# Optimization experiments

Hardware: AMD Instinct MI355X
Metric: run time of the kernel (lower is better)

Reference implementation:

```python
import jax, jax.numpy as jnp
import numpy as np

B, N, C = 4, 1024, 1024
H = 16
D = C // H  # 64
HID = int(int(C * 4.0) * 2 / 3)  # 2730
EPS = 1e-6


def rmsnorm(x, w):
    return x * jax.lax.rsqrt(jnp.mean(x * x, axis=-1, keepdims=True) + EPS) * w


def rope_cos_sin(n, d):
    inv_freq = 1.0 / (10000.0 ** (jnp.arange(0, d, 2, dtype=jnp.float32) / d))
    t = jnp.arange(n, dtype=jnp.float32)
    freqs = jnp.einsum('i,j->ij', t, inv_freq)  # [N, D/2]
    emb = jnp.concatenate([freqs, freqs], axis=-1)  # [N, D]
    return jnp.cos(emb), jnp.sin(emb)


def rotate_half(x):
    x1, x2 = jnp.split(x, 2, axis=-1)
    return jnp.concatenate([-x2, x1], axis=-1)


def setup_inputs() -> dict:
    key = jax.random.key(0)
    ks = jax.random.split(key, 12)
    s = lambda fan_in: 1.0 / np.sqrt(fan_in)
    return {
        'x': jax.random.normal(ks[0], (B, N, C), jnp.float32),
        'c': jax.random.normal(ks[1], (B, C), jnp.float32),
        'norm1_w': jnp.ones((C,), jnp.float32),
        'norm2_w': jnp.ones((C,), jnp.float32),
        'qkv_w': jax.random.normal(ks[2], (C, 3 * C), jnp.float32) * s(C),
        'proj_w': jax.random.normal(ks[3], (C, C), jnp.float32) * s(C),
        'proj_b': jnp.zeros((C,), jnp.float32),
        'qn_w': jnp.ones((D,), jnp.float32),
        'kn_w': jnp.ones((D,), jnp.float32),
        'w1': jax.random.normal(ks[4], (C, HID), jnp.float32) * s(C),
        'w2': jax.random.normal(ks[5], (HID, C), jnp.float32) * s(HID),
        'w3': jax.random.normal(ks[6], (C, HID), jnp.float32) * s(C),
        'ada_w': jax.random.normal(ks[7], (C, 6 * C), jnp.float32) * s(C),
        'ada_b': jnp.zeros((6 * C,), jnp.float32),
    }


def reference(x, c, norm1_w, norm2_w, qkv_w, proj_w, proj_b, qn_w, kn_w, w1, w2, w3, ada_w, ada_b):
    # AdaLN modulation params from conditioning
    mods = jax.nn.silu(c) @ ada_w + ada_b  # [B, 6C]
    sh_msa, sc_msa, g_msa, sh_mlp, sc_mlp, g_mlp = jnp.split(mods, 6, axis=-1)

    # --- attention branch ---
    x_mod = rmsnorm(x, norm1_w) * (1 + sc_msa[:, None, :]) + sh_msa[:, None, :]
    qkv = (x_mod @ qkv_w).reshape(B, N, 3, H, D).transpose(2, 0, 3, 1, 4)  # [3,B,H,N,D]
    q, k, v = qkv[0], qkv[1], qkv[2]
    q = rmsnorm(q, qn_w)
    k = rmsnorm(k, kn_w)
    cos, sin = rope_cos_sin(N, D)  # [N, D]
    q = q * cos + rotate_half(q) * sin
    k = k * cos + rotate_half(k) * sin
    attn = jax.nn.softmax(jnp.einsum('bhqd,bhkd->bhqk', q, k) * (D ** -0.5), axis=-1)
    o = jnp.einsum('bhqk,bhkd->bhqd', attn, v).transpose(0, 2, 1, 3).reshape(B, N, C)
    x = x + g_msa[:, None, :] * (o @ proj_w + proj_b)

    # --- SwiGLU MLP branch ---
    x_mod = rmsnorm(x, norm2_w) * (1 + sc_mlp[:, None, :]) + sh_mlp[:, None, :]
    mlp = (jax.nn.silu(x_mod @ w1) * (x_mod @ w3)) @ w2
    x = x + g_mlp[:, None, :] * mlp
    return x
```

## Files before the change

kernel.cpp:

```cpp
#include <hip/hip_runtime.h>
#include <hip/hip_bf16.h>
#include <stdint.h>

using bf16 = __hip_bfloat16;
using bf16x8 = __attribute__((ext_vector_type(8))) short;
using f32x4  = __attribute__((ext_vector_type(4))) float;
using short4v = __attribute__((ext_vector_type(4))) short;

#define EPSF 1e-6f

__device__ __forceinline__ unsigned short f2bu(float x) {
  union { bf16 h; unsigned short u; } cvt;
  cvt.h = __float2bfloat16(x);
  return cvt.u;
}

typedef __attribute__((address_space(3))) void as3_void;
typedef const __attribute__((address_space(1))) void as1_void;

__device__ __forceinline__ void gload_lds16(const void* g, void* l) {
  as1_void* gp = (as1_void*)(uintptr_t)g;
  as3_void* lp = (as3_void*)(uint32_t)(uintptr_t)l;
  __builtin_amdgcn_global_load_lds(gp, lp, 16, 0, 0);
}

__global__ void rope_tab(float* __restrict__ cosT, float* __restrict__ sinT) {
  const int i = blockIdx.x * 256 + threadIdx.x;
  const int n = i >> 5, fi = i & 31;
  const float invf = powf(10000.f, -(float)fi * (1.f / 32.f));
  const float ang = (float)n * invf;
  cosT[i] = cosf(ang);
  sinT[i] = sinf(ang);
}

__global__ void __launch_bounds__(256) ada_part(const float* __restrict__ cc,
                                                const float* __restrict__ adaw,
                                                float* __restrict__ part) {
  __shared__ float sc[256];
  __shared__ float red[1024];
  const int t = threadIdx.x;
  const int cb = blockIdx.x % 48, ks = blockIdx.x / 48;
  const int k0 = ks * 64;
  {
    const int b = t >> 6, kk = t & 63;
    const float v = cc[b * 1024 + k0 + kk];
    sc[t] = v / (1.f + __expf(-v));
  }
  __syncthreads();
  const int colL = t & 127, kh = t >> 7;
  const int col = cb * 128 + colL;
  float a0 = 0.f, a1 = 0.f, a2 = 0.f, a3 = 0.f;
  const float* ap = adaw + (size_t)(k0 + kh * 32) * 6144 + col;
#pragma unroll
  for (int k = 0; k < 32; ++k) {
    const float awv = ap[(size_t)k * 6144];
    const int kk = kh * 32 + k;
    a0 += sc[kk] * awv; a1 += sc[64 + kk] * awv;
    a2 += sc[128 + kk] * awv; a3 += sc[192 + kk] * awv;
  }
  red[kh * 512 + 0 * 128 + colL] = a0;
  red[kh * 512 + 1 * 128 + colL] = a1;
  red[kh * 512 + 2 * 128 + colL] = a2;
  red[kh * 512 + 3 * 128 + colL] = a3;
  __syncthreads();
  if (kh == 0) {
#pragma unroll
    for (int b = 0; b < 4; ++b) {
      const float s = red[b * 128 + colL] + red[512 + b * 128 + colL];
      part[(size_t)(ks * 4 + b) * 6144 + col] = s;
    }
  }
}

__global__ void __launch_bounds__(256) ada_reduce(const float* __restrict__ part,
                                                  const float* __restrict__ adab,
                                                  float* __restrict__ mods) {
  const int i = blockIdx.x * 256 + threadIdx.x;
  const int b = i / 6144, col = i % 6144;
  float s = adab[col];
#pragma unroll
  for (int ks = 0; ks < 16; ++ks) s += part[(size_t)(ks * 4 + b) * 6144 + col];
  mods[b * 6144 + col] = s;
}

__global__ void __launch_bounds__(256) norm_mod(const float* __restrict__ X,
                                                const float* __restrict__ wgt,
                                                const float* __restrict__ mods,
                                                int sh_off, int sc_off,
                                                bf16* __restrict__ Y) {
  __shared__ float red[4];
  const int row = blockIdx.x, t = threadIdx.x, l = t & 63, wv = t >> 6;
  const float4 xv = ((const float4*)(X + (size_t)row * 1024))[t];
  float ss = xv.x * xv.x + xv.y * xv.y + xv.z * xv.z + xv.w * xv.w;
#pragma unroll
  for (int off = 1; off < 64; off <<= 1) ss += __shfl_xor(ss, off);
  if (l == 0) red[wv] = ss;
  __syncthreads();
  ss = (red[0] + red[1]) + (red[2] + red[3]);
  const float rs = rsqrtf(ss * (1.f / 1024.f) + EPSF);
  const int b = row >> 10;
  const float* mb = mods + b * 6144;
  const int c0 = t * 4;
  float vals[4] = {xv.x, xv.y, xv.z, xv.w};
  short4v yv;
#pragma unroll
  for (int j = 0; j < 4; j++) {
    const int cc = c0 + j;
    const float y = vals[j] * rs * wgt[cc] * (1.f + mb[sc_off + cc]) + mb[sh_off + cc];
    yv[j] = (short)f2bu(y);
  }
  *(short4v*)(Y + (size_t)row * 1024 + c0) = yv;
}

__global__ void __launch_bounds__(256) transpose_all(const float* __restrict__ qkvw,
                                                     const float* __restrict__ projw,
                                                     const float* __restrict__ w1,
                                                     const float* __restrict__ w3,
                                                     const float* __restrict__ w2,
                                                     bf16* __restrict__ qkvwt,
                                                     bf16* __restrict__ projwt,
                                                     bf16* __restrict__ w1t,
                                                     bf16* __restrict__ w3t,
                                                     bf16* __restrict__ w2t) {
  int id = blockIdx.x;
  const float* src; bf16* dst; int R, Cc, ldd, nbx;
  if (id < 3072)      { src = qkvw;  dst = qkvwt;  R = 1024; Cc = 3072; ldd = 1024; nbx = 96; }
  else if ((id -= 3072) < 1024) { src = projw; dst = projwt; R = 1024; Cc = 1024; ldd = 1024; nbx = 32; }
  else if ((id -= 1024) < 2752) { src = w1;    dst = w1t;    R = 1024; Cc = 2730; ldd = 1024; nbx = 86; }
  else if ((id -= 2752) < 2752) { src = w3;    dst = w3t;    R = 1024; Cc = 2730; ldd = 1024; nbx = 86; }
  else                { id -= 2752; src = w2;    dst = w2t;    R = 2730; Cc = 1024; ldd = 2816; nbx = 32; }
  const int bx = id % nbx, by = id / nbx;
  __shared__ float tile[32][33];
  const int tx = threadIdx.x & 31, ty = threadIdx.x >> 5;
  const int ct = bx * 32, rt = by * 32;
#pragma unroll
  for (int kk = 0; kk < 4; ++kk) {
    const int r = rt + ty + kk * 8;
    float v = 0.f;
    if (r < R && (ct + tx) < Cc) v = src[(size_t)r * Cc + ct + tx];
    tile[ty + kk * 8][tx] = v;
  }
  __syncthreads();
#pragma unroll
  for (int kk = 0; kk < 4; ++kk) {
    const int c = ct + ty + kk * 8;
    const int r = rt + tx;
    if (c < Cc && r < ldd) dst[(size_t)c * ldd + r] = __float2bfloat16(tile[tx][ty + kk * 8]);
  }
}

template <int TN, int EPI>
__global__ void __launch_bounds__(256, 3) gemm_p(const bf16* __restrict__ A, int lda,
                                                 const bf16* __restrict__ Bt, int ldb,
                                                 int K, int Nreal, int ldc,
                                                 bf16* __restrict__ outb,
                                                 float* __restrict__ outf,
                                                 const float* __restrict__ resid,
                                                 const float* __restrict__ gate,
                                                 const float* __restrict__ bias) {
  constexpr int BUFSZ = 8192 + TN * 64;
  constexpr int WN = (TN == 128) ? 2 : 1;
  constexpr int MI = (TN == 128) ? 4 : 2;
  constexpr int WTM = (TN == 128) ? 64 : 32;
  __shared__ char smB[3 * BUFSZ];
  const int t = threadIdx.x, l = t & 63, w = t >> 6;
  const int g = l >> 4, cl = l & 15;
  const int cpx = gridDim.x >> 3;
  const int wg = blockIdx.x;
  const int swz0 = (wg & 7) * cpx + (wg >> 3);
  const int m0 = (swz0 & 31) * 128, n0 = (swz0 >> 5) * TN;
  const int wm = w / WN, wn = w % WN;
  f32x4 acc[MI][4] = {};
  const int NK = K >> 5;
  const int srow = t >> 2;
  const int scol = (((t & 3) ^ ((t >> 3) & 3))) * 8;
  const int rsw = (cl >> 1) & 3;

  auto stage = [&](int kt, int buf) {
    char* dst = smB + buf * BUFSZ;
    const int kk = kt * 32 + scol;
    gload_lds16(A + (size_t)(m0 + srow) * lda + kk,      dst + t * 16);
    gload_lds16(A + (size_t)(m0 + 64 + srow) * lda + kk, dst + 4096 + t * 16);
    gload_lds16(Bt + (size_t)(n0 + srow) * ldb + kk,     dst + 8192 + t * 16);
    if constexpr (TN == 128)
      gload_lds16(Bt + (size_t)(n0 + 64 + srow) * ldb + kk, dst + 12288 + t * 16);
  };

  stage(0, 0);
  stage(1, 1);
  if constexpr (TN == 128) asm volatile("s_waitcnt vmcnt(4)" ::: "memory");
  else                     asm volatile("s_waitcnt vmcnt(3)" ::: "memory");
  __builtin_amdgcn_s_barrier();
  __builtin_amdgcn_sched_barrier(0);
  int cur = 0;
  for (int kt = 0; kt < NK; ++kt) {
    if (kt + 2 < NK) stage(kt + 2, (cur >= 1) ? cur - 1 : 2);
    const bf16* Ab = (const bf16*)(smB + cur * BUFSZ);
    const bf16* Bb = (const bf16*)(smB + cur * BUFSZ + 8192);
    bf16x8 af[MI], bfr[4];
#pragma unroll
    for (int i = 0; i < MI; i++)
      af[i] = *(const bf16x8*)&Ab[(wm * WTM + i * 16 + cl) * 32 + ((g ^ rsw) << 3)];
#pragma unroll
    for (int i = 0; i < 4; i++)
      bfr[i] = *(const bf16x8*)&Bb[(wn * 64 + i * 16 + cl) * 32 + ((g ^ rsw) << 3)];
    __builtin_amdgcn_s_setprio(1);
#pragma unroll
    for (int mi = 0; mi < MI; mi++)
#pragma unroll
      for (int ni = 0; ni < 4; ni++)
        acc[mi][ni] = __builtin_amdgcn_mfma_f32_16x16x32_bf16(af[mi], bfr[ni], acc[mi][ni], 0, 0, 0);
    __builtin_amdgcn_s_setprio(0);
    if (kt + 2 < NK) {
      if constexpr (TN == 128) asm volatile("s_waitcnt vmcnt(4)" ::: "memory");
      else                     asm volatile("s_waitcnt vmcnt(3)" ::: "memory");
    } else {
      asm volatile("s_waitcnt vmcnt(0)" ::: "memory");
    }
    __builtin_amdgcn_s_barrier();
    __builtin_amdgcn_sched_barrier(0);
    cur = (cur + 1 == 3) ? 0 : cur + 1;
  }
#pragma unroll
  for (int mi = 0; mi < MI; mi++) {
#pragma unroll
    for (int ni = 0; ni < 4; ni++) {
      const int c = n0 + wn * 64 + ni * 16 + cl;
#pragma unroll
      for (int j = 0; j < 4; j++) {
        const int r = m0 + wm * WTM + mi * 16 + g * 4 + j;
        const float v = acc[mi][ni][j];
        if constexpr (EPI == 0) {
          if (c < Nreal) outb[(size_t)r * ldc + c] = __float2bfloat16(v);
        } else if constexpr (EPI == 1) {
          const int b = r >> 10;
          outf[(size_t)r * ldc + c] = resid[(size_t)r * ldc + c] + gate[b * 6144 + c] * (v + bias[c]);
        } else if constexpr (EPI == 4) {
          const int b = r >> 10;
          outf[(size_t)r * ldc + c] = resid[(size_t)r * ldc + c] + gate[b * 6144 + c] * v;
        }
      }
    }
  }
}

__global__ void __launch_bounds__(256, 3) gemm_qkv(const bf16* __restrict__ A, int lda,
                                                   const bf16* __restrict__ Bt, int ldb,
                                                   const float* __restrict__ cosT,
                                                   const float* __restrict__ sinT,
                                                   const float* __restrict__ qnw,
                                                   const float* __restrict__ knw,
                                                   bf16* __restrict__ Qo,
                                                   bf16* __restrict__ Ko,
                                                   bf16* __restrict__ vbt) {
  constexpr int BUFSZ = 16384;
  __shared__ char smB[3 * BUFSZ];
  const int t = threadIdx.x, l = t & 63, w = t >> 6;
  const int g = l >> 4, cl = l & 15;
  const int cpx = gridDim.x >> 3;
  const int wg = blockIdx.x;
  const int swz0 = (wg & 7) * cpx + (wg >> 3);
  const int m0 = (swz0 & 31) * 128, n0 = (swz0 >> 5) * 128;
  const int wm = w >> 1, wn = w & 1;
  f32x4 acc[4][4] = {};
  const int srow = t >> 2;
  const int scol = (((t & 3) ^ ((t >> 3) & 3))) * 8;
  const int rsw = (cl >> 1) & 3;

  auto stage = [&](int kt, int buf) {
    char* dst = smB + buf * BUFSZ;
    const int kk = kt * 32 + scol;
    gload_lds16(A + (size_t)(m0 + srow) * lda + kk,       dst + t * 16);
    gload_lds16(A + (size_t)(m0 + 64 + srow) * lda + kk,  dst + 4096 + t * 16);
    gload_lds16(Bt + (size_t)(n0 + srow) * ldb + kk,      dst + 8192 + t * 16);
    gload_lds16(Bt + (size_t)(n0 + 64 + srow) * ldb + kk, dst + 12288 + t * 16);
  };

  stage(0, 0);
  stage(1, 1);
  asm volatile("s_waitcnt vmcnt(4)" ::: "memory");
  __builtin_amdgcn_s_barrier();
  __builtin_amdgcn_sched_barrier(0);
  int cur = 0;
  for (int kt = 0; kt < 32; ++kt) {
    if (kt + 2 < 32) stage(kt + 2, (cur >= 1) ? cur - 1 : 2);
    const bf16* Ab = (const bf16*)(smB + cur * BUFSZ);
    const bf16* Bb = (const bf16*)(smB + cur * BUFSZ + 8192);
    bf16x8 af[4], bfr[4];
#pragma unroll
    for (int i = 0; i < 4; i++)
      af[i] = *(const bf16x8*)&Ab[(wm * 64 + i * 16 + cl) * 32 + ((g ^ rsw) << 3)];
#pragma unroll
    for (int i = 0; i < 4; i++)
      bfr[i] = *(const bf16x8*)&Bb[(wn * 64 + i * 16 + cl) * 32 + ((g ^ rsw) << 3)];
    __builtin_amdgcn_s_setprio(1);
#pragma unroll
    for (int mi = 0; mi < 4; mi++)
#pragma unroll
      for (int ni = 0; ni < 4; ni++)
        acc[mi][ni] = __builtin_amdgcn_mfma_f32_16x16x32_bf16(af[mi], bfr[ni], acc[mi][ni], 0, 0, 0);
    __builtin_amdgcn_s_setprio(0);
    if (kt + 2 < 32) asm volatile("s_waitcnt vmcnt(4)" ::: "memory");
    else             asm volatile("s_waitcnt vmcnt(0)" ::: "memory");
    __builtin_amdgcn_s_barrier();
    __builtin_amdgcn_sched_barrier(0);
    cur = (cur + 1 == 3) ? 0 : cur + 1;
  }

  float* cosS = (float*)smB;
  float* sinS = (float*)(smB + 16384);
  const int nb0 = m0 & 1023;
  for (int i = t; i < 4096; i += 256) {
    cosS[i] = cosT[(nb0 + (i >> 5)) * 32 + (i & 31)];
    sinS[i] = sinT[(nb0 + (i >> 5)) * 32 + (i & 31)];
  }
  __syncthreads();

  const int hb = n0 + wn * 64;
  const int type = hb >> 10;
  const int h = (hb & 1023) >> 6;
  const int b = m0 >> 10;
  const int bh = b * 16 + h;

  if (type == 2) {
#pragma unroll
    for (int mi = 0; mi < 4; mi++) {
      const int r0 = m0 + wm * 64 + mi * 16 + g * 4;
      const int nn0 = r0 & 1023;
#pragma unroll
      for (int ni = 0; ni < 4; ni++) {
        const int d = ni * 16 + cl;
        short4v pv;
#pragma unroll
        for (int j = 0; j < 4; j++) pv[j] = (short)f2bu(acc[mi][ni][j]);
        *(short4v*)(vbt + (size_t)bh * 65536 + (size_t)d * 1024 + nn0) = pv;
      }
    }
  } else {
    bf16* dst = (type == 0) ? Qo : Ko;
    const float* nwp = (type == 0) ? qnw : knw;
    const float scale = (type == 0) ? 0.125f : 1.f;
    float wv[4];
#pragma unroll
    for (int ni = 0; ni < 4; ni++) wv[ni] = nwp[ni * 16 + cl];
#pragma unroll
    for (int mi = 0; mi < 4; mi++) {
#pragma unroll
      for (int j = 0; j < 4; j++) {
        float ssq = 0.f;
#pragma unroll
        for (int ni = 0; ni < 4; ni++) ssq += acc[mi][ni][j] * acc[mi][ni][j];
        ssq += __shfl_xor(ssq, 1);
        ssq += __shfl_xor(ssq, 2);
        ssq += __shfl_xor(ssq, 4);
        ssq += __shfl_xor(ssq, 8);
        const float rsn = rsqrtf(ssq * (1.f / 64.f) + EPSF);
        const int r = m0 + wm * 64 + mi * 16 + g * 4 + j;
        const int nn = r & 1023, rr = r - m0;
        float vn[4];
#pragma unroll
        for (int ni = 0; ni < 4; ni++) vn[ni] = acc[mi][ni][j] * rsn * wv[ni];
        const float cs0 = cosS[rr * 32 + cl],      sn0 = sinS[rr * 32 + cl];
        const float cs1 = cosS[rr * 32 + 16 + cl], sn1 = sinS[rr * 32 + 16 + cl];
        const float o0 = (vn[0] * cs0 - vn[2] * sn0) * scale;
        const float o1 = (vn[1] * cs1 - vn[3] * sn1) * scale;
        const float o2 = (vn[2] * cs0 + vn[0] * sn0) * scale;
        const float o3 = (vn[3] * cs1 + vn[1] * sn1) * scale;
        const size_t base = ((size_t)bh * 1024 + nn) * 64;
        dst[base + cl] = __float2bfloat16(o0);
        dst[base + 16 + cl] = __float2bfloat16(o1);
        dst[base + 32 + cl] = __float2bfloat16(o2);
        dst[base + 48 + cl] = __float2bfloat16(o3);
      }
    }
  }
}

__global__ void __launch_bounds__(256, 2) gemm_dual(const bf16* __restrict__ A, int lda,
                                                    const bf16* __restrict__ B1t,
                                                    const bf16* __restrict__ B3t, int ldb,
                                                    int K, int Nreal, int ldc,
                                                    bf16* __restrict__ outb) {
  constexpr int BUFSZ = 24576;
  __shared__ char smB[2 * BUFSZ];
  const int t = threadIdx.x, l = t & 63, w = t >> 6;
  const int g = l >> 4, cl = l & 15;
  const int cpx = gridDim.x >> 3;
  const int wg = blockIdx.x;
  const int swz0 = (wg & 7) * cpx + (wg >> 3);
  const int m0 = (swz0 & 31) * 128, n0 = (swz0 >> 5) * 128;
  const int wm = w >> 1, wn = w & 1;
  f32x4 acc1[4][4] = {}, acc3[4][4] = {};
  const int NK = K >> 5;
  const int srow = t >> 2;
  const int scol = (((t & 3) ^ ((t >> 3) & 3))) * 8;
  const int rsw = (cl >> 1) & 3;

  auto stage = [&](int kt, int buf) {
    char* dst = smB + buf * BUFSZ;
    const int kk = kt * 32 + scol;
    gload_lds16(A   + (size_t)(m0 + srow) * lda + kk,      dst + t * 16);
    gload_lds16(A   + (size_t)(m0 + 64 + srow) * lda + kk, dst + 4096 + t * 16);
    gload_lds16(B1t + (size_t)(n0 + srow) * ldb + kk,      dst + 8192 + t * 16);
    gload_lds16(B1t + (size_t)(n0 + 64 + srow) * ldb + kk, dst + 12288 + t * 16);
    gload_lds16(B3t + (size_t)(n0 + srow) * ldb + kk,      dst + 16384 + t * 16);
    gload_lds16(B3t + (size_t)(n0 + 64 + srow) * ldb + kk, dst + 20480 + t * 16);
  };

  stage(0, 0);
  for (int kt = 0; kt < NK; ++kt) {
    if (kt + 1 < NK) {
      stage(kt + 1, (kt + 1) & 1);
      asm volatile("s_waitcnt vmcnt(6)" ::: "memory");
    } else {
      asm volatile("s_waitcnt vmcnt(0)" ::: "memory");
    }
    __builtin_amdgcn_s_barrier();
    __builtin_amdgcn_sched_barrier(0);
    const bf16* Ab  = (const bf16*)(smB + (kt & 1) * BUFSZ);
    const bf16* B1b = (const bf16*)(smB + (kt & 1) * BUFSZ + 8192);
    const bf16* B3b = (const bf16*)(smB + (kt & 1) * BUFSZ + 16384);
    bf16x8 af[4], b1r[4], b3r[4];
#pragma unroll
    for (int i = 0; i < 4; i++)
      af[i] = *(const bf16x8*)&Ab[(wm * 64 + i * 16 + cl) * 32 + ((g ^ rsw) << 3)];
#pragma unroll
    for (int i = 0; i < 4; i++) {
      b1r[i] = *(const bf16x8*)&B1b[(wn * 64 + i * 16 + cl) * 32 + ((g ^ rsw) << 3)];
      b3r[i] = *(const bf16x8*)&B3b[(wn * 64 + i * 16 + cl) * 32 + ((g ^ rsw) << 3)];
    }
    __builtin_amdgcn_s_setprio(1);
#pragma unroll
    for (int mi = 0; mi < 4; mi++)
#pragma unroll
      for (int ni = 0; ni < 4; ni++) {
        acc1[mi][ni] = __builtin_amdgcn_mfma_f32_16x16x32_bf16(af[mi], b1r[ni], acc1[mi][ni], 0, 0, 0);
        acc3[mi][ni] = __builtin_amdgcn_mfma_f32_16x16x32_bf16(af[mi], b3r[ni], acc3[mi][ni], 0, 0, 0);
      }
    __builtin_amdgcn_s_setprio(0);
    __builtin_amdgcn_s_barrier();
    __builtin_amdgcn_sched_barrier(0);
  }
#pragma unroll
  for (int mi = 0; mi < 4; mi++) {
#pragma unroll
    for (int ni = 0; ni < 4; ni++) {
      const int c = n0 + wn * 64 + ni * 16 + cl;
#pragma unroll
      for (int j = 0; j < 4; j++) {
        const int r = m0 + wm * 64 + mi * 16 + g * 4 + j;
        if (c < Nreal) {
          const float hv = acc1[mi][ni][j];
          const float sl = hv / (1.f + __expf(-hv));
          outb[(size_t)r * ldc + c] = __float2bfloat16(sl * acc3[mi][ni][j]);
        } else {
          outb[(size_t)r * ldc + c] = __float2bfloat16(0.f);
        }
      }
    }
  }
}

__global__ void __launch_bounds__(512) attn_fwd(const bf16* __restrict__ Qb,
                                                const bf16* __restrict__ Kb,
                                                const bf16* __restrict__ Vb,
                                                bf16* __restrict__ Ob) {
  __shared__ char KsB[2 * 8192];
  __shared__ char VsB[2 * 8192];
  __shared__ unsigned short Ps[8 * 16 * 64];
  const int t = threadIdx.x, l = t & 63, w = t >> 6;
  const int g = l >> 4, cl = l & 15;
  const int wg = blockIdx.x;
  const int bh = wg & 63;
  const int q0 = (wg >> 6) * 128;
  const bf16* Qg = Qb + (size_t)bh * 65536;
  const bf16* Kg = Kb + (size_t)bh * 65536;
  const bf16* Vg = Vb + (size_t)bh * 65536;
  const int qrow = q0 + w * 16 + cl;
  const bf16x8 aq0 = *(const bf16x8*)(Qg + (size_t)qrow * 64 + g * 8);
  const bf16x8 aq1 = *(const bf16x8*)(Qg + (size_t)qrow * 64 + 32 + g * 8);
  float mreg = -1e30f, lreg = 0.f;
  f32x4 o[4] = {};
  const int kr_l = t >> 3;
  const int ku = (t & 7) ^ ((t >> 3) & 7);
  unsigned short* Pw = Ps + w * 1024;
  const int sxor = cl & 7;

  auto stageKV = [&](int kvt, int buf) {
    const int kv0 = kvt * 64;
    gload_lds16(Kg + (size_t)(kv0 + kr_l) * 64 + ku * 8, KsB + buf * 8192 + w * 1024);
    gload_lds16(Vg + (size_t)kr_l * 1024 + kv0 + ku * 8, VsB + buf * 8192 + w * 1024);
  };

  stageKV(0, 0);
  for (int kvt = 0; kvt < 16; ++kvt) {
    const int cb = kvt & 1;
    if (kvt + 1 < 16) {
      stageKV(kvt + 1, cb ^ 1);
      asm volatile("s_waitcnt vmcnt(2)" ::: "memory");
    } else {
      asm volatile("s_waitcnt vmcnt(0)" ::: "memory");
    }
    __builtin_amdgcn_s_barrier();
    __builtin_amdgcn_sched_barrier(0);
    const char* Kt = KsB + cb * 8192;
    const char* Vt = VsB + cb * 8192;
    f32x4 s[4] = {};
#pragma unroll
    for (int ch = 0; ch < 4; ch++) {
      const int rb = (16 * ch + cl) << 7;
      const bf16x8 bk0 = *(const bf16x8*)(Kt + rb + ((g ^ sxor) << 4));
      s[ch] = __builtin_amdgcn_mfma_f32_16x16x32_bf16(bk0, aq0, s[ch], 0, 0, 0);
      const bf16x8 bk1 = *(const bf16x8*)(Kt + rb + (((4 + g) ^ sxor) << 4));
      s[ch] = __builtin_amdgcn_mfma_f32_16x16x32_bf16(bk1, aq1, s[ch], 0, 0, 0);
    }
    float pm = fmaxf(fmaxf(fmaxf(s[0][0], s[0][1]), fmaxf(s[0][2], s[0][3])),
                     fmaxf(fmaxf(s[1][0], s[1][1]), fmaxf(s[1][2], s[1][3])));
    pm = fmaxf(pm, fmaxf(fmaxf(fmaxf(s[2][0], s[2][1]), fmaxf(s[2][2], s[2][3])),
                         fmaxf(fmaxf(s[3][0], s[3][1]), fmaxf(s[3][2], s[3][3]))));
    pm = fmaxf(pm, __shfl_xor(pm, 16));
    pm = fmaxf(pm, __shfl_xor(pm, 32));
    const float nm = fmaxf(mreg, pm);
    const float al = __expf(mreg - nm);
    mreg = nm;
    float rs = 0.f;
#pragma unroll
    for (int ch = 0; ch < 4; ch++) {
      const float p0 = __expf(s[ch][0] - nm);
      const float p1 = __expf(s[ch][1] - nm);
      const float p2 = __expf(s[ch][2] - nm);
      const float p3 = __expf(s[ch][3] - nm);
      rs += (p0 + p1) + (p2 + p3);
      short4v pk;
      pk[0] = (short)f2bu(p0); pk[1] = (short)f2bu(p1);
      pk[2] = (short)f2bu(p2); pk[3] = (short)f2bu(p3);
      const int phys = (2 * ch + (g >> 1)) ^ sxor;
      *(short4v*)&Pw[cl * 64 + phys * 8 + 4 * (g & 1)] = pk;
    }
    rs += __shfl_xor(rs, 16);
    rs += __shfl_xor(rs, 32);
    lreg = lreg * al + rs;
#pragma unroll
    for (int dc = 0; dc < 4; dc++) {
      o[dc][0] *= al; o[dc][1] *= al; o[dc][2] *= al; o[dc][3] *= al;
    }
    const bf16x8 pa0 = *(const bf16x8*)&Pw[cl * 64 + ((g ^ sxor) << 3)];
    const bf16x8 pa1 = *(const bf16x8*)&Pw[cl * 64 + (((4 + g) ^ sxor) << 3)];
#pragma unroll
    for (int dc = 0; dc < 4; dc++) {
      const int vr = (16 * dc + cl) << 7;
      const bf16x8 bv0 = *(const bf16x8*)(Vt + vr + ((g ^ sxor) << 4));
      o[dc] = __builtin_amdgcn_mfma_f32_16x16x32_bf16(bv0, pa0, o[dc], 0, 0, 0);
      const bf16x8 bv1 = *(const bf16x8*)(Vt + vr + (((4 + g) ^ sxor) << 4));
      o[dc] = __builtin_amdgcn_mfma_f32_16x16x32_bf16(bv1, pa1, o[dc], 0, 0, 0);
    }
    __builtin_amdgcn_s_barrier();
  }
  const int b = bh >> 4, h = bh & 15;
  const float inv = 1.f / lreg;
  const int q = q0 + w * 16 + cl;
  const size_t base = ((size_t)(b * 1024 + q) * 16 + h) * 64;
#pragma unroll
  for (int dc = 0; dc < 4; dc++) {
    short4v ov;
    ov[0] = (short)f2bu(o[dc][0] * inv);
    ov[1] = (short)f2bu(o[dc][1] * inv);
    ov[2] = (short)f2bu(o[dc][2] * inv);
    ov[3] = (short)f2bu(o[dc][3] * inv);
    *(short4v*)(Ob + base + 16 * dc + 4 * g) = ov;
  }
}

extern "C" void kernel_launch(void* const* d_in, const int* in_sizes, int n_in,
                              void* d_out, int out_size, void* d_ws, size_t ws_size,
                              hipStream_t stream) {
  const float* x     = (const float*)d_in[0];
  const float* c     = (const float*)d_in[1];
  const float* n1w   = (const float*)d_in[2];
  const float* n2w   = (const float*)d_in[3];
  const float* qkvw  = (const float*)d_in[4];
  const float* projw = (const float*)d_in[5];
  const float* projb = (const float*)d_in[6];
  const float* qnw   = (const float*)d_in[7];
  const float* knw   = (const float*)d_in[8];
  const float* w1    = (const float*)d_in[9];
  const float* w2    = (const float*)d_in[10];
  const float* w3    = (const float*)d_in[11];
  const float* adaw  = (const float*)d_in[12];
  const float* adab  = (const float*)d_in[13];
  float* outp = (float*)d_out;
  char* ws = (char*)d_ws;
  if (ws_size < 93159424u) return;

  float* ropeC = (float*)(ws + 0);
  float* ropeS = (float*)(ws + 131072);
  float* mods  = (float*)(ws + 262144);
  bf16* xmod   = (bf16*)(ws + 360448);
  bf16* qkvwt  = (bf16*)(ws + 8749056);
  bf16* projwt = (bf16*)(ws + 15040512);
  bf16* w1t    = (bf16*)(ws + 17137664);
  bf16* w3t    = (bf16*)(ws + 22904832);
  bf16* w2t    = (bf16*)(ws + 28672000);
  float* apart = (float*)(ws + 34439168);
  bf16* qb     = (bf16*)(ws + 59604992);
  bf16* gbuf   = (bf16*)(ws + 59604992);
  bf16* kb     = (bf16*)(ws + 67993600);
  bf16* vbt    = (bf16*)(ws + 76382208);
  bf16* ob     = (bf16*)(ws + 84770816);

  rope_tab<<<128, 256, 0, stream>>>(ropeC, ropeS);
  ada_part<<<768, 256, 0, stream>>>(c, adaw, apart);
  ada_reduce<<<96, 256, 0, stream>>>(apart, adab, mods);
  transpose_all<<<12416, 256, 0, stream>>>(qkvw, projw, w1, w3, w2,
                                           qkvwt, projwt, w1t, w3t, w2t);

  norm_mod<<<4096, 256, 0, stream>>>(x, n1w, mods, 0, 1024, xmod);
  gemm_qkv<<<768, 256, 0, stream>>>(xmod, 1024, qkvwt, 1024, ropeC, ropeS, qnw, knw,
                                    qb, kb, vbt);
  attn_fwd<<<512, 512, 0, stream>>>(qb, kb, vbt, ob);
  gemm_p<64, 1><<<512, 256, 0, stream>>>(ob, 1024, projwt, 1024, 1024, 1024, 1024,
                                         nullptr, outp, x, mods + 2048, projb);

  norm_mod<<<4096, 256, 0, stream>>>(outp, n2w, mods, 3072, 4096, xmod);
  gemm_dual<<<704, 256, 0, stream>>>(xmod, 1024, w1t, w3t, 1024, 1024, 2730, 2816,
                                     gbuf);
  gemm_p<64, 4><<<512, 256, 0, stream>>>(gbuf, 2816, w2t, 2816, 2816, 1024, 1024,
                                         nullptr, outp, outp, mods + 5120, nullptr);
}
```

Measured before the change: 233.9 us.

## Fuse preamble kernels and use exp2 softmax with lazy rescaling

Merges the rope table, adaLN partial matmul and weight transpose/convert kernels into one launch, removing two kernel launches and their serialization gaps. In attention, the log2(e) factor is folded into the Q scale so exp2f replaces __expf. The online-softmax rescale of the accumulator and row sum is skipped unless the running max rises by more than 8 in log2 units. This lazy rescale removes per-iteration multiplies, but lets probabilities reach up to 2^8 before bf16 packing, which could slightly affect accuracy.

```diff
diff --git a/kernel.cpp b/kernel.cpp
--- a/kernel.cpp
+++ b/kernel.cpp
@@ -8,6 +8,7 @@
 using short4v = __attribute__((ext_vector_type(4))) short;
 
 #define EPSF 1e-6f
+#define LOG2E 1.44269504088896f
 
 __device__ __forceinline__ unsigned short f2bu(float x) {
   union { bf16 h; unsigned short u; } cvt;
@@ -24,51 +25,90 @@
   __builtin_amdgcn_global_load_lds(gp, lp, 16, 0, 0);
 }
 
-__global__ void rope_tab(float* __restrict__ cosT, float* __restrict__ sinT) {
-  const int i = blockIdx.x * 256 + threadIdx.x;
-  const int n = i >> 5, fi = i & 31;
-  const float invf = powf(10000.f, -(float)fi * (1.f / 32.f));
-  const float ang = (float)n * invf;
-  cosT[i] = cosf(ang);
-  sinT[i] = sinf(ang);
-}
-
-__global__ void __launch_bounds__(256) ada_part(const float* __restrict__ cc,
+__global__ void __launch_bounds__(256) preamble(const float* __restrict__ qkvw,
+                                                const float* __restrict__ projw,
+                                                const float* __restrict__ w1,
+                                                const float* __restrict__ w3,
+                                                const float* __restrict__ w2,
+                                                bf16* __restrict__ qkvwt,
+                                                bf16* __restrict__ projwt,
+                                                bf16* __restrict__ w1t,
+                                                bf16* __restrict__ w3t,
+                                                bf16* __restrict__ w2t,
+                                                const float* __restrict__ cc,
                                                 const float* __restrict__ adaw,
-                                                float* __restrict__ part) {
+                                                float* __restrict__ part,
+                                                float* __restrict__ cosT,
+                                                float* __restrict__ sinT) {
+  __shared__ float tile[32][33];
   __shared__ float sc[256];
   __shared__ float red[1024];
+  int id = blockIdx.x;
   const int t = threadIdx.x;
-  const int cb = blockIdx.x % 48, ks = blockIdx.x / 48;
-  const int k0 = ks * 64;
-  {
-    const int b = t >> 6, kk = t & 63;
-    const float v = cc[b * 1024 + k0 + kk];
-    sc[t] = v / (1.f + __expf(-v));
-  }
-  __syncthreads();
-  const int colL = t & 127, kh = t >> 7;
-  const int col = cb * 128 + colL;
-  float a0 = 0.f, a1 = 0.f, a2 = 0.f, a3 = 0.f;
-  const float* ap = adaw + (size_t)(k0 + kh * 32) * 6144 + col;
-#pragma unroll
-  for (int k = 0; k < 32; ++k) {
-    const float awv = ap[(size_t)k * 6144];
-    const int kk = kh * 32 + k;
-    a0 += sc[kk] * awv; a1 += sc[64 + kk] * awv;
-    a2 += sc[128 + kk] * awv; a3 += sc[192 + kk] * awv;
-  }
-  red[kh * 512 + 0 * 128 + colL] = a0;
-  red[kh * 512 + 1 * 128 + colL] = a1;
-  red[kh * 512 + 2 * 128 + colL] = a2;
-  red[kh * 512 + 3 * 128 + colL] = a3;
-  __syncthreads();
-  if (kh == 0) {
-#pragma unroll
-    for (int b = 0; b < 4; ++b) {
-      const float s = red[b * 128 + colL] + red[512 + b * 128 + colL];
-      part[(size_t)(ks * 4 + b) * 6144 + col] = s;
-    }
+  if (id < 12416) {
+    const float* src; bf16* dst; int R, Cc, ldd, nbx;
+    if (id < 3072)      { src = qkvw;  dst = qkvwt;  R = 1024; Cc = 3072; ldd = 1024; nbx = 96; }
+    else if ((id -= 3072) < 1024) { src = projw; dst = projwt; R = 1024; Cc = 1024; ldd = 1024; nbx = 32; }
+    else if ((id -= 1024) < 2752) { src = w1;    dst = w1t;    R = 1024; Cc = 2730; ldd = 1024; nbx = 86; }
+    else if ((id -= 2752) < 2752) { src = w3;    dst = w3t;    R = 1024; Cc = 2730; ldd = 1024; nbx = 86; }
+    else                { id -= 2752; src = w2;    dst = w2t;    R = 2730; Cc = 1024; ldd = 2816; nbx = 32; }
+    const int bx = id % nbx, by = id / nbx;
+    const int tx = t & 31, ty = t >> 5;
+    const int ct = bx * 32, rt = by * 32;
+#pragma unroll
+    for (int kk = 0; kk < 4; ++kk) {
+      const int r = rt + ty + kk * 8;
+      float v = 0.f;
+      if (r < R && (ct + tx) < Cc) v = src[(size_t)r * Cc + ct + tx];
+      tile[ty + kk * 8][tx] = v;
+    }
+    __syncthreads();
+#pragma unroll
+    for (int kk = 0; kk < 4; ++kk) {
+      const int c = ct + ty + kk * 8;
+      const int r = rt + tx;
+      if (c < Cc && r < ldd) dst[(size_t)c * ldd + r] = __float2bfloat16(tile[tx][ty + kk * 8]);
+    }
+  } else if ((id -= 12416) < 768) {
+    const int cb = id % 48, ks = id / 48;
+    const int k0 = ks * 64;
+    {
+      const int b = t >> 6, kk = t & 63;
+      const float v = cc[b * 1024 + k0 + kk];
+      sc[t] = v / (1.f + __expf(-v));
+    }
+    __syncthreads();
+    const int colL = t & 127, kh = t >> 7;
+    const int col = cb * 128 + colL;
+    float a0 = 0.f, a1 = 0.f, a2 = 0.f, a3 = 0.f;
+    const float* ap = adaw + (size_t)(k0 + kh * 32) * 6144 + col;
+#pragma unroll
+    for (int k = 0; k < 32; ++k) {
+      const float awv = ap[(size_t)k * 6144];
+      const int kk = kh * 32 + k;
+      a0 += sc[kk] * awv; a1 += sc[64 + kk] * awv;
+      a2 += sc[128 + kk] * awv; a3 += sc[192 + kk] * awv;
+    }
+    red[kh * 512 + 0 * 128 + colL] = a0;
+    red[kh * 512 + 1 * 128 + colL] = a1;
+    red[kh * 512 + 2 * 128 + colL] = a2;
+    red[kh * 512 + 3 * 128 + colL] = a3;
+    __syncthreads();
+    if (kh == 0) {
+#pragma unroll
+      for (int b = 0; b < 4; ++b) {
+        const float s = red[b * 128 + colL] + red[512 + b * 128 + colL];
+        part[(size_t)(ks * 4 + b) * 6144 + col] = s;
+      }
+    }
+  } else {
+    id -= 768;
+    const int i = id * 256 + t;
+    const int n = i >> 5, fi = i & 31;
+    const float invf = powf(10000.f, -(float)fi * (1.f / 32.f));
+    const float ang = (float)n * invf;
+    cosT[i] = cosf(ang);
+    sinT[i] = sinf(ang);
   }
 }
 
@@ -110,43 +150,6 @@
     yv[j] = (short)f2bu(y);
   }
   *(short4v*)(Y + (size_t)row * 1024 + c0) = yv;
-}
-
-__global__ void __launch_bounds__(256) transpose_all(const float* __restrict__ qkvw,
-                                                     const float* __restrict__ projw,
-                                                     const float* __restrict__ w1,
-                                                     const float* __restrict__ w3,
-                                                     const float* __restrict__ w2,
-                                                     bf16* __restrict__ qkvwt,
-                                                     bf16* __restrict__ projwt,
-                                                     bf16* __restrict__ w1t,
-                                                     bf16* __restrict__ w3t,
-                                                     bf16* __restrict__ w2t) {
-  int id = blockIdx.x;
-  const float* src; bf16* dst; int R, Cc, ldd, nbx;
-  if (id < 3072)      { src = qkvw;  dst = qkvwt;  R = 1024; Cc = 3072; ldd = 1024; nbx = 96; }
-  else if ((id -= 3072) < 1024) { src = projw; dst = projwt; R = 1024; Cc = 1024; ldd = 1024; nbx = 32; }
-  else if ((id -= 1024) < 2752) { src = w1;    dst = w1t;    R = 1024; Cc = 2730; ldd = 1024; nbx = 86; }
-  else if ((id -= 2752) < 2752) { src = w3;    dst = w3t;    R = 1024; Cc = 2730; ldd = 1024; nbx = 86; }
-  else                { id -= 2752; src = w2;    dst = w2t;    R = 2730; Cc = 1024; ldd = 2816; nbx = 32; }
-  const int bx = id % nbx, by = id / nbx;
-  __shared__ float tile[32][33];
-  const int tx = threadIdx.x & 31, ty = threadIdx.x >> 5;
-  const int ct = bx * 32, rt = by * 32;
-#pragma unroll
-  for (int kk = 0; kk < 4; ++kk) {
-    const int r = rt + ty + kk * 8;
-    float v = 0.f;
-    if (r < R && (ct + tx) < Cc) v = src[(size_t)r * Cc + ct + tx];
-    tile[ty + kk * 8][tx] = v;
-  }
-  __syncthreads();
-#pragma unroll
-  for (int kk = 0; kk < 4; ++kk) {
-    const int c = ct + ty + kk * 8;
-    const int r = rt + tx;
-    if (c < Cc && r < ldd) dst[(size_t)c * ldd + r] = __float2bfloat16(tile[tx][ty + kk * 8]);
-  }
 }
 
 template <int TN, int EPI>
@@ -339,7 +342,7 @@
   } else {
     bf16* dst = (type == 0) ? Qo : Ko;
     const float* nwp = (type == 0) ? qnw : knw;
-    const float scale = (type == 0) ? 0.125f : 1.f;
+    const float scale = (type == 0) ? 0.125f * LOG2E : 1.f;
     float wv[4];
 #pragma unroll
     for (int ni = 0; ni < 4; ni++) wv[ni] = nwp[ni * 16 + cl];
@@ -520,16 +523,23 @@
                          fmaxf(fmaxf(s[3][0], s[3][1]), fmaxf(s[3][2], s[3][3]))));
     pm = fmaxf(pm, __shfl_xor(pm, 16));
     pm = fmaxf(pm, __shfl_xor(pm, 32));
-    const float nm = fmaxf(mreg, pm);
-    const float al = __expf(mreg - nm);
-    mreg = nm;
+    if (!__all(pm - mreg <= 8.f)) {
+      const float nm = fmaxf(mreg, pm);
+      const float al = exp2f(mreg - nm);
+      mreg = nm;
+      lreg *= al;
+#pragma unroll
+      for (int dc = 0; dc < 4; dc++) {
+        o[dc][0] *= al; o[dc][1] *= al; o[dc][2] *= al; o[dc][3] *= al;
+      }
+    }
     float rs = 0.f;
 #pragma unroll
     for (int ch = 0; ch < 4; ch++) {
-      const float p0 = __expf(s[ch][0] - nm);
-      const float p1 = __expf(s[ch][1] - nm);
-      const float p2 = __expf(s[ch][2] - nm);
-      const float p3 = __expf(s[ch][3] - nm);
+      const float p0 = exp2f(s[ch][0] - mreg);
+      const float p1 = exp2f(s[ch][1] - mreg);
+      const float p2 = exp2f(s[ch][2] - mreg);
+      const float p3 = exp2f(s[ch][3] - mreg);
       rs += (p0 + p1) + (p2 + p3);
       short4v pk;
       pk[0] = (short)f2bu(p0); pk[1] = (short)f2bu(p1);
@@ -539,11 +549,7 @@
     }
     rs += __shfl_xor(rs, 16);
     rs += __shfl_xor(rs, 32);
-    lreg = lreg * al + rs;
-#pragma unroll
-    for (int dc = 0; dc < 4; dc++) {
-      o[dc][0] *= al; o[dc][1] *= al; o[dc][2] *= al; o[dc][3] *= al;
-    }
+    lreg += rs;
     const bf16x8 pa0 = *(const bf16x8*)&Pw[cl * 64 + ((g ^ sxor) << 3)];
     const bf16x8 pa1 = *(const bf16x8*)&Pw[cl * 64 + (((4 + g) ^ sxor) << 3)];
 #pragma unroll
@@ -608,11 +614,10 @@
   bf16* vbt    = (bf16*)(ws + 76382208);
   bf16* ob     = (bf16*)(ws + 84770816);
 
-  rope_tab<<<128, 256, 0, stream>>>(ropeC, ropeS);
-  ada_part<<<768, 256, 0, stream>>>(c, adaw, apart);
+  preamble<<<13312, 256, 0, stream>>>(qkvw, projw, w1, w3, w2,
+                                      qkvwt, projwt, w1t, w3t, w2t,
+                                      c, adaw, apart, ropeC, ropeS);
   ada_reduce<<<96, 256, 0, stream>>>(apart, adab, mods);
-  transpose_all<<<12416, 256, 0, stream>>>(qkvw, projw, w1, w3, w2,
-                                           qkvwt, projwt, w1t, w3t, w2t);
 
   norm_mod<<<4096, 256, 0, stream>>>(x, n1w, mods, 0, 1024, xmod);
   gemm_qkv<<<768, 256, 0, stream>>>(xmod, 1024, qkvwt, 1024, ropeC, ropeS, qnw, knw,
```

Measured after the change: 231.9 us, median of 2. No clear change (-0.9%).
